# Kernel tuning notes

Measured on AMD Instinct MI355X. Metric: run time of the kernel, lower is better.

The kernel has to match this reference:

```python
import jax, jax.numpy as jnp
import numpy as np
from jax import lax

B, C, H, W = 16, 128, 64, 64
O, K, KS = 128, 4, 3
R = max(C // 4, 1)  # reduced channels in SE branch


def setup_inputs() -> dict:
    key = jax.random.key(0)
    ks = jax.random.split(key, 6)
    x = jax.random.normal(ks[0], (B, C, H, W), dtype=jnp.float32)
    # SE-style weight generator: 1x1 convs == linears on pooled features
    w1 = jax.random.normal(ks[1], (R, C), dtype=jnp.float32) * (1.0 / np.sqrt(C))
    b1 = jnp.zeros((R,), dtype=jnp.float32)
    w2 = jax.random.normal(ks[2], (K, R), dtype=jnp.float32) * (1.0 / np.sqrt(R))
    b2 = jnp.zeros((K,), dtype=jnp.float32)
    # bank of conv kernels, torch init is randn
    kernels = jax.random.normal(ks[3], (K, O, C, KS, KS), dtype=jnp.float32)
    return {"x": x, "w1": w1, "b1": b1, "w2": w2, "b2": b2, "kernels": kernels}


def reference(x, w1, b1, w2, b2, kernels):
    b = x.shape[0]
    # --- attention over kernels (SE branch) ---
    pooled = jnp.mean(x, axis=(2, 3))                    # (B, C)
    h = jax.nn.relu(pooled @ w1.T + b1)                  # (B, R)
    attn = jax.nn.softmax(h @ w2.T + b2, axis=1)         # (B, K)
    # --- all K convolutions fused into one conv with K*O output channels ---
    k, o, c, kh, kw = kernels.shape
    wflat = kernels.reshape(k * o, c, kh, kw)
    pad = (kh - 1) // 2
    conv = lax.conv_general_dilated(
        x, wflat,
        window_strides=(1, 1),
        padding=[(pad, pad), (pad, pad)],
        dimension_numbers=("NCHW", "OIHW", "NCHW"),
    )                                                    # (B, K*O, H, W)
    conv = conv.reshape(b, k, o, conv.shape[2], conv.shape[3])
    # per-sample weighted sum over the kernel bank
    out = jnp.einsum("bk,bkohw->bohw", attn, conv)       # (B, O, H, W)
    return out
```

## Files before the change

kernel.cpp:

```cpp
#include <hip/hip_runtime.h>

#define BB 16
#define CC 128
#define HH 64
#define WW 64
#define OO 128
#define KK 4
#define RR 32
#define KTOT 1152
#define NT 36
#define XP 66

typedef short v8s __attribute__((ext_vector_type(8)));
typedef float v4f __attribute__((ext_vector_type(4)));

__device__ __forceinline__ unsigned short f2bf(float f) {
    unsigned u = __builtin_bit_cast(unsigned, f);
    u += 0x7fffu + ((u >> 16) & 1u);
    return (unsigned short)(u >> 16);
}

__device__ __forceinline__ void gl16(const unsigned short* g, unsigned short* l) {
    __builtin_amdgcn_global_load_lds(
        (const __attribute__((address_space(1))) unsigned int*)g,
        (__attribute__((address_space(3))) unsigned int*)l, 16, 0, 0);
}

__global__ void border_kernel(unsigned short* __restrict__ xbp, float* __restrict__ pooled) {
    int b = blockIdx.y;
    if (blockIdx.x == 0 && threadIdx.x < CC) pooled[b * CC + threadIdx.x] = 0.f;
    int i = blockIdx.x * 256 + threadIdx.x;
    if (i >= 4160) return;
    int cell = i >> 4, wi = i & 15;
    int r, c;
    if (cell < 66)       { r = 0;              c = cell; }
    else if (cell < 132) { r = 65;             c = cell - 66; }
    else if (cell < 196) { r = cell - 132 + 1; c = 0; }
    else                 { r = cell - 196 + 1; c = 65; }
    *(v8s*)(xbp + ((size_t)((b * XP + r) * XP + c)) * CC + wi * 8) = (v8s)0;
}

__global__ __launch_bounds__(256) void convert_pool_kernel(const float* __restrict__ x,
        unsigned short* __restrict__ xbp, float* __restrict__ pooled) {
    int idx = blockIdx.x * 256 + threadIdx.x;
    int p = idx & 4095;
    int g = (idx >> 12) & 15;
    int b = idx >> 16;
    const float* xp = x + ((size_t)(b * CC + g * 8)) * 4096 + p;
    float vals[8];
    v8s v;
    #pragma unroll
    for (int j = 0; j < 8; ++j) {
        vals[j] = xp[(size_t)j * 4096];
        v[j] = (short)f2bf(vals[j]);
    }
    int h = p >> 6, w = p & 63;
    *(v8s*)(xbp + ((size_t)((b * XP + h + 1) * XP + w + 1)) * CC + g * 8) = v;

    __shared__ float ls[4][8];
    int lane = threadIdx.x & 63, wv = threadIdx.x >> 6;
    #pragma unroll
    for (int j = 0; j < 8; ++j) {
        float s = vals[j];
        #pragma unroll
        for (int off = 32; off > 0; off >>= 1) s += __shfl_down(s, off, 64);
        if (lane == 0) ls[wv][j] = s;
    }
    __syncthreads();
    if (threadIdx.x < 8) {
        float s = ls[0][threadIdx.x] + ls[1][threadIdx.x] + ls[2][threadIdx.x] + ls[3][threadIdx.x];
        atomicAdd(&pooled[b * CC + g * 8 + threadIdx.x], s);
    }
}

__global__ __launch_bounds__(256) void mix_kernel(const float* __restrict__ kernels,
        const float* __restrict__ pooled,
        const float* __restrict__ w1, const float* __restrict__ b1,
        const float* __restrict__ w2, const float* __restrict__ b2,
        unsigned short* __restrict__ wmixb) {
    const int b = blockIdx.y, o = blockIdx.x;
    const int t = threadIdx.x;
    __shared__ float hs[RR];
    __shared__ float lgs[KK];
    __shared__ float attns[KK];
    __shared__ unsigned short ws[KTOT];

    if (t < RR) {
        float acc = b1[t];
        const float* pr = pooled + b * CC;
        const float* wr = w1 + t * CC;
        for (int c = 0; c < CC; ++c) acc += (pr[c] * (1.0f / 4096.0f)) * wr[c];
        hs[t] = fmaxf(acc, 0.f);
    }
    __syncthreads();
    if (t < KK) {
        float a = b2[t];
        #pragma unroll
        for (int r = 0; r < RR; ++r) a += hs[r] * w2[t * RR + r];
        lgs[t] = a;
    }
    __syncthreads();
    if (t == 0) {
        float m = fmaxf(fmaxf(lgs[0], lgs[1]), fmaxf(lgs[2], lgs[3]));
        float e0 = expf(lgs[0] - m), e1 = expf(lgs[1] - m);
        float e2 = expf(lgs[2] - m), e3 = expf(lgs[3] - m);
        float inv = 1.f / (e0 + e1 + e2 + e3);
        attns[0] = e0 * inv; attns[1] = e1 * inv; attns[2] = e2 * inv; attns[3] = e3 * inv;
    }
    __syncthreads();
    float a0 = attns[0], a1 = attns[1], a2 = attns[2], a3 = attns[3];

    const size_t KB = (size_t)OO * KTOT;
    const float* k0 = kernels + (size_t)o * KTOT;
    for (int ii = t; ii < KTOT; ii += 256) {
        int c = ii / 9, tap = ii - c * 9;
        float v = a0 * k0[ii] + a1 * k0[KB + ii] + a2 * k0[2 * KB + ii] + a3 * k0[3 * KB + ii];
        ws[tap * 128 + c] = f2bf(v);
    }
    __syncthreads();
    v8s* wp8 = (v8s*)(wmixb + ((size_t)b * OO + o) * KTOT);
    const v8s* ls8 = (const v8s*)ws;
    for (int ii = t; ii < KTOT / 8; ii += 256) wp8[ii] = ls8[ii];
}

#define MFMA16(acc, va, vb) \
    asm volatile("v_mfma_f32_16x16x32_bf16 %0, %1, %2, %0" : "+v"(acc) : "v"(va), "v"(vb))

#define STAGE(ks_, buf_) { \
    const int tap_ = (ks_) >> 2; \
    const int dy_ = tap_ / 3, dx_ = tap_ % 3; \
    const int c0_ = ((ks_) & 3) * 32; \
    const unsigned short* sa_ = srcA0 + (ks_) * 32; \
    const unsigned short* sb_ = srcB0 + ((size_t)(dy_ * XP + dx_)) * CC + c0_; \
    gl16(sa_,                     &Ab[buf_][wid * 512]); \
    gl16(sa_ + (size_t)64 * KTOT, &Ab[buf_][(wid + 4) * 512]); \
    gl16(sb_,                     &Bb[buf_][wid * 512]); \
    gl16(sb_ + XP * CC,           &Bb[buf_][(wid + 4) * 512]); \
}

__global__ __launch_bounds__(256, 2) void conv_kernel(
        const unsigned short* __restrict__ xbp,
        const unsigned short* __restrict__ wmixb,
        float* __restrict__ out) {
    __shared__ unsigned short Ab[2][4096];
    __shared__ unsigned short Bb[2][4096];
    int bid = blockIdx.x;
    int xcd = bid & 7, idx = bid >> 3;
    int b = xcd * 2 + (idx >> 5);
    int nt = idx & 31;
    int t = threadIdx.x;
    int lane = t & 63, wid = t >> 6;
    int wm = wid & 1, wn = wid >> 1;

    v4f acc[4][4];
    #pragma unroll
    for (int i = 0; i < 4; ++i)
        #pragma unroll
        for (int j = 0; j < 4; ++j) acc[i][j] = (v4f)0.f;

    int l4 = lane >> 2, g = lane & 3;
    const unsigned short* srcA0 = wmixb + ((size_t)(b * OO + wid * 16 + l4)) * KTOT + g * 8;
    const unsigned short* srcB0 = xbp + ((size_t)((b * XP + nt * 2) * XP) + wid * 16 + l4) * CC + g * 8;
    int lane_off = (lane & 15) * 64 + (lane >> 4) * 16;

    STAGE(0, 0);
    asm volatile("s_waitcnt vmcnt(0)" ::: "memory");
    __syncthreads();

    #pragma unroll
    for (int ks = 0; ks < NT; ++ks) {
        const int buf_ = ks & 1;
        if (ks < NT - 1) STAGE(ks + 1, buf_ ^ 1);
        v8s af[4], bfv[4];
        const char* abase = (const char*)&Ab[buf_][0] + wm * 4096 + lane_off;
        const char* bbase = (const char*)&Bb[buf_][0] + wn * 4096 + lane_off;
        #pragma unroll
        for (int mf = 0; mf < 4; ++mf) af[mf] = *(const v8s*)(abase + mf * 1024);
        #pragma unroll
        for (int nf = 0; nf < 4; ++nf) bfv[nf] = *(const v8s*)(bbase + nf * 1024);
        #pragma unroll
        for (int mf = 0; mf < 4; ++mf)
            #pragma unroll
            for (int nf = 0; nf < 4; ++nf)
                MFMA16(acc[mf][nf], af[mf], bfv[nf]);
        asm volatile("s_waitcnt vmcnt(0)" ::: "memory");
        __syncthreads();
    }
    asm volatile("s_nop 7\ns_nop 7" ::: );

    int r = nt * 2 + wn;
    #pragma unroll
    for (int mf = 0; mf < 4; ++mf) {
        int o = wm * 64 + mf * 16 + ((lane >> 4) << 2);
        #pragma unroll
        for (int jj = 0; jj < 4; ++jj) {
            float* op = out + (((size_t)(b * OO + o + jj)) * HH + r) * WW;
            #pragma unroll
            for (int nf = 0; nf < 4; ++nf)
                op[nf * 16 + (lane & 15)] = acc[mf][nf][jj];
        }
    }
}

extern "C" void kernel_launch(void* const* d_in, const int* in_sizes, int n_in,
                              void* d_out, int out_size, void* d_ws, size_t ws_size,
                              hipStream_t stream) {
    const float* x       = (const float*)d_in[0];
    const float* w1      = (const float*)d_in[1];
    const float* b1      = (const float*)d_in[2];
    const float* w2      = (const float*)d_in[3];
    const float* b2      = (const float*)d_in[4];
    const float* kernels = (const float*)d_in[5];
    float* out = (float*)d_out;

    float* pooled = (float*)d_ws;
    unsigned short* xbp   = (unsigned short*)(pooled + BB * CC);
    unsigned short* wmixb = xbp + (size_t)BB * XP * XP * CC;

    border_kernel<<<dim3(17, BB), 256, 0, stream>>>(xbp, pooled);
    convert_pool_kernel<<<4096, 256, 0, stream>>>(x, xbp, pooled);
    mix_kernel<<<dim3(OO, BB), 256, 0, stream>>>(kernels, pooled, w1, b1, w2, b2, wmixb);
    conv_kernel<<<512, 256, 0, stream>>>(xbp, wmixb, out);
}
```

Before: 65.10 us.

## Triple-buffer conv staging, fold border zeroing into convert, drop pooling atomics

The conv kernel moves from a double-buffered to a triple-buffered LDS pipeline. It prefetches two stages ahead and waits with a partial vmcnt, so each k-step needs one barrier instead of a full drain. The separate border-zeroing kernel is removed: edge threads of the convert kernel now write the padding zeros. Pooling atomics are replaced by per-block partial sums, which the mix kernel reduces in shared memory. This cuts one launch and the atomic contention, at the cost of more LDS per block, which may lower occupancy.

```diff
diff --git a/kernel.cpp b/kernel.cpp
--- a/kernel.cpp
+++ b/kernel.cpp
@@ -26,26 +26,13 @@
         (__attribute__((address_space(3))) unsigned int*)l, 16, 0, 0);
 }
 
-__global__ void border_kernel(unsigned short* __restrict__ xbp, float* __restrict__ pooled) {
-    int b = blockIdx.y;
-    if (blockIdx.x == 0 && threadIdx.x < CC) pooled[b * CC + threadIdx.x] = 0.f;
-    int i = blockIdx.x * 256 + threadIdx.x;
-    if (i >= 4160) return;
-    int cell = i >> 4, wi = i & 15;
-    int r, c;
-    if (cell < 66)       { r = 0;              c = cell; }
-    else if (cell < 132) { r = 65;             c = cell - 66; }
-    else if (cell < 196) { r = cell - 132 + 1; c = 0; }
-    else                 { r = cell - 196 + 1; c = 65; }
-    *(v8s*)(xbp + ((size_t)((b * XP + r) * XP + c)) * CC + wi * 8) = (v8s)0;
-}
-
 __global__ __launch_bounds__(256) void convert_pool_kernel(const float* __restrict__ x,
-        unsigned short* __restrict__ xbp, float* __restrict__ pooled) {
-    int idx = blockIdx.x * 256 + threadIdx.x;
-    int p = idx & 4095;
-    int g = (idx >> 12) & 15;
-    int b = idx >> 16;
+        unsigned short* __restrict__ xbp, float* __restrict__ part) {
+    int bid = blockIdx.x;
+    int t = threadIdx.x;
+    int p = (bid & 15) * 256 + t;
+    int g = (bid >> 4) & 15;
+    int b = bid >> 8;
     const float* xp = x + ((size_t)(b * CC + g * 8)) * 4096 + p;
     float vals[8];
     v8s v;
@@ -55,10 +42,21 @@
         v[j] = (short)f2bf(vals[j]);
     }
     int h = p >> 6, w = p & 63;
-    *(v8s*)(xbp + ((size_t)((b * XP + h + 1) * XP + w + 1)) * CC + g * 8) = v;
+    unsigned short* xb_b = xbp + (size_t)b * XP * XP * CC + g * 8;
+    *(v8s*)(xb_b + (size_t)((h + 1) * XP + w + 1) * CC) = v;
+
+    v8s z = (v8s)0;
+    if (w == 0)  *(v8s*)(xb_b + (size_t)((h + 1) * XP) * CC) = z;
+    if (w == 63) *(v8s*)(xb_b + (size_t)((h + 1) * XP + 65) * CC) = z;
+    if (h == 0)  *(v8s*)(xb_b + (size_t)(w + 1) * CC) = z;
+    if (h == 63) *(v8s*)(xb_b + (size_t)(65 * XP + w + 1) * CC) = z;
+    if (h == 0 && w == 0)   *(v8s*)(xb_b + 0) = z;
+    if (h == 0 && w == 63)  *(v8s*)(xb_b + (size_t)65 * CC) = z;
+    if (h == 63 && w == 0)  *(v8s*)(xb_b + (size_t)(65 * XP) * CC) = z;
+    if (h == 63 && w == 63) *(v8s*)(xb_b + (size_t)(65 * XP + 65) * CC) = z;
 
     __shared__ float ls[4][8];
-    int lane = threadIdx.x & 63, wv = threadIdx.x >> 6;
+    int lane = t & 63, wv = t >> 6;
     #pragma unroll
     for (int j = 0; j < 8; ++j) {
         float s = vals[j];
@@ -67,29 +65,37 @@
         if (lane == 0) ls[wv][j] = s;
     }
     __syncthreads();
-    if (threadIdx.x < 8) {
-        float s = ls[0][threadIdx.x] + ls[1][threadIdx.x] + ls[2][threadIdx.x] + ls[3][threadIdx.x];
-        atomicAdd(&pooled[b * CC + g * 8 + threadIdx.x], s);
+    if (t < 8) {
+        float s = ls[0][t] + ls[1][t] + ls[2][t] + ls[3][t];
+        part[(((b * 16 + g) * 16) + (bid & 15)) * 8 + t] = s;
     }
 }
 
 __global__ __launch_bounds__(256) void mix_kernel(const float* __restrict__ kernels,
-        const float* __restrict__ pooled,
+        const float* __restrict__ part,
         const float* __restrict__ w1, const float* __restrict__ b1,
         const float* __restrict__ w2, const float* __restrict__ b2,
         unsigned short* __restrict__ wmixb) {
     const int b = blockIdx.y, o = blockIdx.x;
     const int t = threadIdx.x;
+    __shared__ float pooled_sh[CC];
     __shared__ float hs[RR];
     __shared__ float lgs[KK];
     __shared__ float attns[KK];
     __shared__ unsigned short ws[KTOT];
 
+    if (t < CC) {
+        const float* pp = part + ((b * 16 + (t >> 3)) * 16) * 8 + (t & 7);
+        float s = 0.f;
+        #pragma unroll
+        for (int pb = 0; pb < 16; ++pb) s += pp[pb * 8];
+        pooled_sh[t] = s * (1.0f / 4096.0f);
+    }
+    __syncthreads();
     if (t < RR) {
         float acc = b1[t];
-        const float* pr = pooled + b * CC;
         const float* wr = w1 + t * CC;
-        for (int c = 0; c < CC; ++c) acc += (pr[c] * (1.0f / 4096.0f)) * wr[c];
+        for (int c = 0; c < CC; ++c) acc += pooled_sh[c] * wr[c];
         hs[t] = fmaxf(acc, 0.f);
     }
     __syncthreads();
@@ -142,8 +148,8 @@
         const unsigned short* __restrict__ xbp,
         const unsigned short* __restrict__ wmixb,
         float* __restrict__ out) {
-    __shared__ unsigned short Ab[2][4096];
-    __shared__ unsigned short Bb[2][4096];
+    __shared__ unsigned short Ab[3][4096];
+    __shared__ unsigned short Bb[3][4096];
     int bid = blockIdx.x;
     int xcd = bid & 7, idx = bid >> 3;
     int b = xcd * 2 + (idx >> 5);
@@ -164,13 +170,18 @@
     int lane_off = (lane & 15) * 64 + (lane >> 4) * 16;
 
     STAGE(0, 0);
-    asm volatile("s_waitcnt vmcnt(0)" ::: "memory");
-    __syncthreads();
+    STAGE(1, 1);
 
     #pragma unroll
     for (int ks = 0; ks < NT; ++ks) {
-        const int buf_ = ks & 1;
-        if (ks < NT - 1) STAGE(ks + 1, buf_ ^ 1);
+        if (ks == NT - 1) {
+            asm volatile("s_waitcnt vmcnt(0)" ::: "memory");
+        } else {
+            asm volatile("s_waitcnt vmcnt(4)" ::: "memory");
+        }
+        __builtin_amdgcn_s_barrier();
+        if (ks + 2 < NT) STAGE(ks + 2, (ks + 2) % 3);
+        const int buf_ = ks % 3;
         v8s af[4], bfv[4];
         const char* abase = (const char*)&Ab[buf_][0] + wm * 4096 + lane_off;
         const char* bbase = (const char*)&Bb[buf_][0] + wn * 4096 + lane_off;
@@ -183,8 +194,6 @@
             #pragma unroll
             for (int nf = 0; nf < 4; ++nf)
                 MFMA16(acc[mf][nf], af[mf], bfv[nf]);
-        asm volatile("s_waitcnt vmcnt(0)" ::: "memory");
-        __syncthreads();
     }
     asm volatile("s_nop 7\ns_nop 7" ::: );
 
@@ -213,12 +222,11 @@
     const float* kernels = (const float*)d_in[5];
     float* out = (float*)d_out;
 
-    float* pooled = (float*)d_ws;
-    unsigned short* xbp   = (unsigned short*)(pooled + BB * CC);
+    float* part = (float*)d_ws;
+    unsigned short* xbp   = (unsigned short*)(part + 16 * 16 * 16 * 8);
     unsigned short* wmixb = xbp + (size_t)BB * XP * XP * CC;
 
-    border_kernel<<<dim3(17, BB), 256, 0, stream>>>(xbp, pooled);
-    convert_pool_kernel<<<4096, 256, 0, stream>>>(x, xbp, pooled);
-    mix_kernel<<<dim3(OO, BB), 256, 0, stream>>>(kernels, pooled, w1, b1, w2, b2, wmixb);
+    convert_pool_kernel<<<4096, 256, 0, stream>>>(x, xbp, part);
+    mix_kernel<<<dim3(OO, BB), 256, 0, stream>>>(kernels, part, w1, b1, w2, b2, wmixb);
     conv_kernel<<<512, 256, 0, stream>>>(xbp, wmixb, out);
 }
```

New measurement: 58.87 us. 9.6% less time.
